# Performance work log

Measured on AMD Instinct MI355X. Metric: run time of the kernel, lower is better.

The kernel has to match this reference:

```python
import jax, jax.numpy as jnp
import numpy as np

B, L, C, H = 4, 2048, 1024, 16
D = C // H
MAX_SCALE_MUL = float(np.log(100.0))
EPS = 1e-12


def setup_inputs() -> dict:
    key = jax.random.key(0)
    ks = jax.random.split(key, 7)
    return {
        "x": jax.random.normal(ks[0], (B, L, C), dtype=jnp.float32),
        "W_qkv": jax.random.normal(ks[1], (3 * C, C), dtype=jnp.float32) * (C ** -0.5),
        "q_bias": jax.random.normal(ks[2], (C,), dtype=jnp.float32) * 0.02,
        "v_bias": jax.random.normal(ks[3], (C,), dtype=jnp.float32) * 0.02,
        "scale_mul_log": jnp.full((1, H, 1, 1), np.log(4.0), dtype=jnp.float32),
        "W_proj": jax.random.normal(ks[4], (C, C), dtype=jnp.float32) * (C ** -0.5),
        "b_proj": jax.random.normal(ks[5], (C,), dtype=jnp.float32) * 0.02,
    }


def reference(x, W_qkv, q_bias, v_bias, scale_mul_log, W_proj, b_proj):
    Bb, Ll, Cc = x.shape
    # fused QKV projection with bias = cat(q_bias, zeros, v_bias)
    bias = jnp.concatenate([q_bias, jnp.zeros_like(q_bias), v_bias])
    qkv = (x @ W_qkv.T + bias).reshape(Bb, Ll, 3, H, D)
    q, k, v = (jnp.transpose(qkv[:, :, i], (0, 2, 1, 3)) for i in range(3))  # [B,H,L,D]
    # L2-norm attention: normalize q,k; learned per-head scale on q (clamped)
    scale_mul = jnp.exp(jnp.minimum(scale_mul_log, MAX_SCALE_MUL))  # [1,H,1,1]
    q = q / jnp.maximum(jnp.linalg.norm(q, axis=-1, keepdims=True), EPS) * scale_mul
    k = k / jnp.maximum(jnp.linalg.norm(k, axis=-1, keepdims=True), EPS)
    # SDPA with scale=1 (attn_l2_norm path), no mask, no dropout (eval)
    scores = jnp.einsum("bhqd,bhkd->bhqk", q, k)
    attn = jax.nn.softmax(scores, axis=-1)
    out = jnp.einsum("bhqk,bhkd->bhqd", attn, v)
    out = jnp.transpose(out, (0, 2, 1, 3)).reshape(Bb, Ll, Cc)
    return out @ W_proj.T + b_proj
```

## Files before the change

### kernel.cpp

```cpp
#include <hip/hip_runtime.h>
#include <hip/hip_bf16.h>


typedef __attribute__((ext_vector_type(8))) short bf16x8;
typedef __attribute__((ext_vector_type(4))) float f32x4;
typedef __attribute__((ext_vector_type(16))) float f32x16;

#define MAXLOG 4.60517018598809f
#define LOG2E  1.4426950408889634f

__device__ __forceinline__ float bf2f(unsigned short u) {
    union { unsigned int i; float f; } v; v.i = ((unsigned int)u) << 16; return v.f;
}
__device__ __forceinline__ unsigned short f2bf(float f) {
    union { float f; unsigned int i; } v; v.f = f;
    unsigned int x = v.i;
    return (unsigned short)((x + 0x7FFFu + ((x >> 16) & 1u)) >> 16);
}
__device__ __forceinline__ unsigned fbits(float f) {
    union { float f; unsigned u; } v; v.f = f; return v.u;
}
__device__ __forceinline__ bf16x8 pack8(const float* __restrict__ p) {
    float4 a = *(const float4*)p;
    float4 b = *(const float4*)(p + 4);
    bf16x8 r;
    r[0] = (short)f2bf(a.x); r[1] = (short)f2bf(a.y);
    r[2] = (short)f2bf(a.z); r[3] = (short)f2bf(a.w);
    r[4] = (short)f2bf(b.x); r[5] = (short)f2bf(b.y);
    r[6] = (short)f2bf(b.z); r[7] = (short)f2bf(b.w);
    return r;
}
__device__ __forceinline__ void gload_lds16(const void* g, void* l) {
    __builtin_amdgcn_global_load_lds((const __attribute__((address_space(1))) void*)g,
                                     (__attribute__((address_space(3))) void*)l, 16, 0, 0);
}

__global__ __launch_bounds__(256) void k_prep(
    const float* __restrict__ x, const float* __restrict__ Wqkv,
    const float* __restrict__ Wp, const float* __restrict__ qbia,
    const float* __restrict__ vbia,
    unsigned short* __restrict__ xb, unsigned short* __restrict__ Wqkvb,
    unsigned short* __restrict__ Wpb, float* __restrict__ bias3)
{
    int i = blockIdx.x * 256 + threadIdx.x;
    if (i < 1048576) {
        *(bf16x8*)&xb[(long)i * 8] = pack8(&x[(long)i * 8]);
    } else if (i < 1441792) {
        int j = i - 1048576;
        *(bf16x8*)&Wqkvb[(long)j * 8] = pack8(&Wqkv[(long)j * 8]);
    } else if (i < 1572864) {
        int j = i - 1441792;
        *(bf16x8*)&Wpb[(long)j * 8] = pack8(&Wp[(long)j * 8]);
    } else if (i < 1573248) {
        int j = (i - 1572864) * 8;
        for (int u = 0; u < 8; ++u) {
            int n = j + u;
            float v = 0.0f;
            if (n < 1024) v = qbia[n];
            else if (n >= 2048) v = vbia[n - 2048];
            bias3[n] = v;
        }
    }
}

template<bool OUT_F32>
__global__ __launch_bounds__(256) void k_gemm_lds(
    const unsigned short* __restrict__ A, const unsigned short* __restrict__ Bh,
    const float* __restrict__ bias, void* __restrict__ Cp, int N, int K)
{
    __shared__ unsigned short As[128 * 32];
    __shared__ unsigned short Bs[128 * 32];
    const int t = threadIdx.x, wave = t >> 6, lane = t & 63;
    const int quad = lane >> 4, l16 = lane & 15;
    const int bm = blockIdx.x * 128, bn = blockIdx.y * 128;
    const int wr = (wave >> 1) * 64, wc = (wave & 1) * 64;
    f32x4 acc[4][4] = {};

    const int srow = lane >> 2;
    const int scol = (lane & 3) * 8;
    const int c0 = wave * 2, c1 = wave * 2 + 1;
    const long ga0 = (long)(bm + c0 * 16 + srow) * K + scol;
    const long ga1 = (long)(bm + c1 * 16 + srow) * K + scol;
    const long gb0 = (long)(bn + c0 * 16 + srow) * K + scol;
    const long gb1 = (long)(bn + c1 * 16 + srow) * K + scol;

    for (int kt = 0; kt < K; kt += 32) {
        __syncthreads();
        gload_lds16(&A[ga0 + kt], &As[c0 * 512]);
        gload_lds16(&A[ga1 + kt], &As[c1 * 512]);
        gload_lds16(&Bh[gb0 + kt], &Bs[c0 * 512]);
        gload_lds16(&Bh[gb1 + kt], &Bs[c1 * 512]);
        __syncthreads();
        bf16x8 af[4], bfr[4];
        for (int i = 0; i < 4; ++i)
            af[i] = *(const bf16x8*)&As[(wr + i * 16 + l16) * 32 + quad * 8];
        for (int j = 0; j < 4; ++j)
            bfr[j] = *(const bf16x8*)&Bs[(wc + j * 16 + l16) * 32 + quad * 8];
        for (int i = 0; i < 4; ++i)
            for (int j = 0; j < 4; ++j)
                acc[i][j] = __builtin_amdgcn_mfma_f32_16x16x32_bf16(af[i], bfr[j], acc[i][j], 0, 0, 0);
    }
    for (int j = 0; j < 4; ++j) {
        int gn = bn + wc + j * 16 + l16;
        float bv = bias[gn];
        for (int i = 0; i < 4; ++i) {
            int gm0 = bm + wr + i * 16 + quad * 4;
            for (int r = 0; r < 4; ++r) {
                float val = acc[i][j][r] + bv;
                if (OUT_F32) ((float*)Cp)[(long)(gm0 + r) * N + gn] = val;
                else ((unsigned short*)Cp)[(long)(gm0 + r) * N + gn] = f2bf(val);
            }
        }
    }
}

__global__ __launch_bounds__(256) void k_prep_kv(
    const unsigned short* __restrict__ qkv, unsigned short* __restrict__ kb,
    unsigned short* __restrict__ vT)
{
    __shared__ unsigned short Vsh[64 * 72];
    const int t = threadIdx.x;
    const int bh = blockIdx.y, l0 = blockIdx.x * 64;
    const int h = bh & 15, b = bh >> 4;
    const int ll = t >> 2, c16 = (t & 3) * 16;
    const long rowbase = (long)(b * 2048 + l0 + ll) * 3072;

    {
        bf16x8 k0 = *(const bf16x8*)&qkv[rowbase + 1024 + h * 64 + c16];
        bf16x8 k1 = *(const bf16x8*)&qkv[rowbase + 1024 + h * 64 + c16 + 8];
        float e[16]; float ss = 0.f;
        for (int j = 0; j < 8; ++j) { e[j]     = bf2f((unsigned short)k0[j]); ss += e[j] * e[j]; }
        for (int j = 0; j < 8; ++j) { e[8 + j] = bf2f((unsigned short)k1[j]); ss += e[8 + j] * e[8 + j]; }
        ss += __shfl_xor(ss, 1, 64);
        ss += __shfl_xor(ss, 2, 64);
        float rs = 1.0f / fmaxf(sqrtf(ss), 1e-12f);
        bf16x8 o0, o1;
        for (int j = 0; j < 8; ++j) o0[j] = (short)f2bf(e[j] * rs);
        for (int j = 0; j < 8; ++j) o1[j] = (short)f2bf(e[8 + j] * rs);
        long dst = ((long)bh * 2048 + l0 + ll) * 64 + c16;
        *(bf16x8*)&kb[dst]     = o0;
        *(bf16x8*)&kb[dst + 8] = o1;
    }
    *(bf16x8*)&Vsh[ll * 72 + c16]     = *(const bf16x8*)&qkv[rowbase + 2048 + h * 64 + c16];
    *(bf16x8*)&Vsh[ll * 72 + c16 + 8] = *(const bf16x8*)&qkv[rowbase + 2048 + h * 64 + c16 + 8];
    __syncthreads();
    const int d = t >> 2, ls = (t & 3) * 16;
    unsigned short tmp[16];
    for (int j = 0; j < 16; ++j) tmp[j] = Vsh[(ls + j) * 72 + d];
    long dst = (long)(bh * 64 + d) * 2048 + l0 + ls;
    *(bf16x8*)&vT[dst]     = *(bf16x8*)&tmp[0];
    *(bf16x8*)&vT[dst + 8] = *(bf16x8*)&tmp[8];
}

__global__ __launch_bounds__(256, 4) void k_attn32(
    const unsigned short* __restrict__ qkv, const unsigned short* __restrict__ kb,
    const unsigned short* __restrict__ vT, const float* __restrict__ sml,
    unsigned short* __restrict__ attn)
{
    __shared__ unsigned short Ks[2][64 * 72];
    __shared__ unsigned short Vs[2][64 * 72];
    const int t = threadIdx.x, wave = t >> 6, lane = t & 63;
    const int m32 = lane & 31, half = lane >> 5;
    const int bh = blockIdx.y, h = bh & 15, b = bh >> 4;
    const int q0 = blockIdx.x * 128 + wave * 32;
    const float scale = __expf(fminf(sml[h], MAXLOG));
    const float c2 = scale * LOG2E;

    const int qd = m32 >> 2, lo = qd & 3;
    const int prow = ((((lo == 1) || (lo == 2)) ? (qd ^ 3) : qd) << 2) | (m32 & 3);

    bf16x8 aq[4];
    {
        long base = (long)(b * 2048 + q0 + m32) * 3072 + h * 64;
        float e[32]; float ss = 0.f;
        for (int f = 0; f < 4; ++f) {
            aq[f] = *(const bf16x8*)&qkv[base + f * 16 + half * 8];
            for (int j = 0; j < 8; ++j) { float x = bf2f((unsigned short)aq[f][j]); e[f * 8 + j] = x; ss += x * x; }
        }
        ss += __shfl_xor(ss, 32, 64);
        float rs = scale / fmaxf(sqrtf(ss), 1e-12f);
        for (int f = 0; f < 4; ++f)
            for (int j = 0; j < 8; ++j) aq[f][j] = (short)f2bf(e[f * 8 + j] * rs);
    }

    f32x16 o0 = {}, o1 = {}, lacc = {};
    bf16x8 ones; for (int i = 0; i < 8; ++i) ones[i] = (short)0x3F80;
    const int sr = t >> 2, sc = (t & 3) * 16;
    const long kbase = (long)bh * 2048 * 64;
    const long vbase = (long)bh * 64 * 2048;

#define LOADT(kt) \
    kpA = *(const bf16x8*)&kb[kbase + (long)((kt) + sr) * 64 + sc];      \
    kpB = *(const bf16x8*)&kb[kbase + (long)((kt) + sr) * 64 + sc + 8];  \
    vpA = *(const bf16x8*)&vT[vbase + (long)sr * 2048 + (kt) + sc];      \
    vpB = *(const bf16x8*)&vT[vbase + (long)sr * 2048 + (kt) + sc + 8];

#define STORET(buf) \
    *(bf16x8*)&Ks[buf][sr * 72 + sc]     = kpA;  \
    *(bf16x8*)&Ks[buf][sr * 72 + sc + 8] = kpB;  \
    *(bf16x8*)&Vs[buf][sr * 72 + sc]     = vpA;  \
    *(bf16x8*)&Vs[buf][sr * 72 + sc + 8] = vpB;

#define ATTN_STEP(KS, VS) \
    for (int ktile = 0; ktile < 2; ++ktile) {                                             \
        f32x16 s = {};                                                                    \
        for (int f = 0; f < 4; ++f) {                                                     \
            bf16x8 bk = *(const bf16x8*)&KS[(ktile * 32 + prow) * 72 + f * 16 + half * 8];\
            s = __builtin_amdgcn_mfma_f32_32x32x16_bf16(bk, aq[f], s, 0, 0, 0);           \
        }                                                                                 \
        unsigned pu[16];                                                                  \
        for (int j = 0; j < 8; ++j) {                                                     \
            pu[j]     = fbits(__builtin_amdgcn_exp2f(s[j]     * LOG2E - c2));             \
            pu[8 + j] = fbits(__builtin_amdgcn_exp2f(s[8 + j] * LOG2E - c2));             \
        }                                                                                 \
        uint4 a0u, a1u;                                                                   \
        a0u.x = __builtin_amdgcn_perm(pu[1],  pu[0],  0x07060302u);                       \
        a0u.y = __builtin_amdgcn_perm(pu[3],  pu[2],  0x07060302u);                       \
        a0u.z = __builtin_amdgcn_perm(pu[5],  pu[4],  0x07060302u);                       \
        a0u.w = __builtin_amdgcn_perm(pu[7],  pu[6],  0x07060302u);                       \
        a1u.x = __builtin_amdgcn_perm(pu[9],  pu[8],  0x07060302u);                       \
        a1u.y = __builtin_amdgcn_perm(pu[11], pu[10], 0x07060302u);                       \
        a1u.z = __builtin_amdgcn_perm(pu[13], pu[12], 0x07060302u);                       \
        a1u.w = __builtin_amdgcn_perm(pu[15], pu[14], 0x07060302u);                       \
        bf16x8 ap0, ap1;                                                                  \
        __builtin_memcpy(&ap0, &a0u, 16); __builtin_memcpy(&ap1, &a1u, 16);               \
        for (int c = 0; c < 2; ++c) {                                                     \
            bf16x8 apc = c ? ap1 : ap0;                                                   \
            bf16x8 bv0 = *(const bf16x8*)&VS[m32 * 72        + ktile * 32 + c * 16 + half * 8]; \
            bf16x8 bv1 = *(const bf16x8*)&VS[(32 + m32) * 72 + ktile * 32 + c * 16 + half * 8]; \
            o0   = __builtin_amdgcn_mfma_f32_32x32x16_bf16(apc, bv0, o0, 0, 0, 0);        \
            o1   = __builtin_amdgcn_mfma_f32_32x32x16_bf16(apc, bv1, o1, 0, 0, 0);        \
            lacc = __builtin_amdgcn_mfma_f32_32x32x16_bf16(apc, ones, lacc, 0, 0, 0);     \
        }                                                                                 \
    }

    bf16x8 kpA, kpB, vpA, vpB;
    LOADT(0)
    STORET(0)
    __syncthreads();

    for (int kt = 0; kt < 2048; kt += 128) {
        LOADT(kt + 64)
        ATTN_STEP(Ks[0], Vs[0])
        STORET(1)
        __syncthreads();
        const bool more = (kt + 128) < 2048;
        if (more) { LOADT(kt + 128) }
        ATTN_STEP(Ks[1], Vs[1])
        if (more) {
            STORET(0)
            __syncthreads();
        }
    }
#undef LOADT
#undef STORET
#undef ATTN_STEP

    for (int r = 0; r < 16; ++r) {
        int m = (r & 3) + 8 * (r >> 2) + 4 * half;
        float inv = 1.0f / lacc[r];
        long dst = (long)(b * 2048 + q0 + m) * 1024 + h * 64;
        attn[dst + m32]      = f2bf(o0[r] * inv);
        attn[dst + 32 + m32] = f2bf(o1[r] * inv);
    }
}

extern "C" void kernel_launch(void* const* d_in, const int* in_sizes, int n_in,
                              void* d_out, int out_size, void* d_ws, size_t ws_size,
                              hipStream_t stream) {
    const float* x    = (const float*)d_in[0];
    const float* Wqkv = (const float*)d_in[1];
    const float* qbia = (const float*)d_in[2];
    const float* vbia = (const float*)d_in[3];
    const float* sml  = (const float*)d_in[4];
    const float* Wp   = (const float*)d_in[5];
    const float* bp   = (const float*)d_in[6];

    char* ws = (char*)d_ws;
    unsigned short* qkv   = (unsigned short*)ws;
    unsigned short* kbuf  = (unsigned short*)(ws + 50331648);
    unsigned short* Wqkvb = kbuf;
    unsigned short* vT    = (unsigned short*)(ws + 67108864);
    unsigned short* xb    = vT;
    unsigned short* attnb = (unsigned short*)(ws + 83886080);
    float*          bias3 = (float*)(ws + 100663296);
    unsigned short* Wpb   = (unsigned short*)(ws + 100679680);
    float*          out   = (float*)d_out;

    hipLaunchKernelGGL(k_prep, dim3(6146), dim3(256), 0, stream,
                       x, Wqkv, Wp, qbia, vbia, xb, Wqkvb, Wpb, bias3);
    hipLaunchKernelGGL((k_gemm_lds<false>), dim3(64, 24), dim3(256), 0, stream,
                       xb, Wqkvb, bias3, (void*)qkv, 3072, 1024);
    hipLaunchKernelGGL(k_prep_kv, dim3(32, 64), dim3(256), 0, stream, qkv, kbuf, vT);
    hipLaunchKernelGGL(k_attn32, dim3(16, 64), dim3(256), 0, stream, qkv, kbuf, vT, sml, attnb);
    hipLaunchKernelGGL((k_gemm_lds<true>), dim3(64, 8), dim3(256), 0, stream,
                       attnb, Wpb, bp, (void*)out, 1024, 1024);
}
```

Baseline: 299.0 us.

## Use 32x32 MFMA in GEMM, fold log2e into q, split score accumulators

The projection GEMM moves from 16x16x32 MFMA tiles to 32x32x16 tiles with a 2x2 accumulator layout per wave, which cuts LDS fragment reads per MFMA. In attention, log2(e) is folded into the normalized q scale so the exp2 argument needs no per-element multiply. The max subtraction is skipped when the scale is small, since scores are bounded by the scale after L2 normalization. The QK dot product now uses two independent accumulators to shorten the MFMA dependency chain. Rounding log2e into bf16 q adds a small precision cost.

```diff
diff --git a/kernel.cpp b/kernel.cpp
--- a/kernel.cpp
+++ b/kernel.cpp
@@ -3,7 +3,6 @@
 
 
 typedef __attribute__((ext_vector_type(8))) short bf16x8;
-typedef __attribute__((ext_vector_type(4))) float f32x4;
 typedef __attribute__((ext_vector_type(16))) float f32x16;
 
 #define MAXLOG 4.60517018598809f
@@ -71,10 +70,10 @@
     __shared__ unsigned short As[128 * 32];
     __shared__ unsigned short Bs[128 * 32];
     const int t = threadIdx.x, wave = t >> 6, lane = t & 63;
-    const int quad = lane >> 4, l16 = lane & 15;
+    const int m32 = lane & 31, half = lane >> 5;
     const int bm = blockIdx.x * 128, bn = blockIdx.y * 128;
     const int wr = (wave >> 1) * 64, wc = (wave & 1) * 64;
-    f32x4 acc[4][4] = {};
+    f32x16 acc[2][2] = {};
 
     const int srow = lane >> 2;
     const int scol = (lane & 3) * 8;
@@ -91,27 +90,30 @@
         gload_lds16(&Bh[gb0 + kt], &Bs[c0 * 512]);
         gload_lds16(&Bh[gb1 + kt], &Bs[c1 * 512]);
         __syncthreads();
-        bf16x8 af[4], bfr[4];
-        for (int i = 0; i < 4; ++i)
-            af[i] = *(const bf16x8*)&As[(wr + i * 16 + l16) * 32 + quad * 8];
-        for (int j = 0; j < 4; ++j)
-            bfr[j] = *(const bf16x8*)&Bs[(wc + j * 16 + l16) * 32 + quad * 8];
-        for (int i = 0; i < 4; ++i)
-            for (int j = 0; j < 4; ++j)
-                acc[i][j] = __builtin_amdgcn_mfma_f32_16x16x32_bf16(af[i], bfr[j], acc[i][j], 0, 0, 0);
-    }
-    for (int j = 0; j < 4; ++j) {
-        int gn = bn + wc + j * 16 + l16;
-        float bv = bias[gn];
-        for (int i = 0; i < 4; ++i) {
-            int gm0 = bm + wr + i * 16 + quad * 4;
-            for (int r = 0; r < 4; ++r) {
-                float val = acc[i][j][r] + bv;
-                if (OUT_F32) ((float*)Cp)[(long)(gm0 + r) * N + gn] = val;
-                else ((unsigned short*)Cp)[(long)(gm0 + r) * N + gn] = f2bf(val);
+        bf16x8 af[2][2], bfr[2][2];
+        for (int mt = 0; mt < 2; ++mt)
+            for (int f = 0; f < 2; ++f)
+                af[mt][f] = *(const bf16x8*)&As[(wr + mt * 32 + m32) * 32 + f * 16 + half * 8];
+        for (int nt = 0; nt < 2; ++nt)
+            for (int f = 0; f < 2; ++f)
+                bfr[nt][f] = *(const bf16x8*)&Bs[(wc + nt * 32 + m32) * 32 + f * 16 + half * 8];
+        for (int f = 0; f < 2; ++f)
+            for (int mt = 0; mt < 2; ++mt)
+                for (int nt = 0; nt < 2; ++nt)
+                    acc[mt][nt] = __builtin_amdgcn_mfma_f32_32x32x16_bf16(
+                        af[mt][f], bfr[nt][f], acc[mt][nt], 0, 0, 0);
+    }
+    for (int mt = 0; mt < 2; ++mt)
+        for (int nt = 0; nt < 2; ++nt) {
+            int gn = bn + wc + nt * 32 + m32;
+            float bv = bias[gn];
+            for (int r = 0; r < 16; ++r) {
+                int gm = bm + wr + mt * 32 + (r & 3) + 8 * (r >> 2) + 4 * half;
+                float val = acc[mt][nt][r] + bv;
+                if (OUT_F32) ((float*)Cp)[(long)gm * N + gn] = val;
+                else ((unsigned short*)Cp)[(long)gm * N + gn] = f2bf(val);
             }
         }
-    }
 }
 
 __global__ __launch_bounds__(256) void k_prep_kv(
@@ -178,7 +180,7 @@
             for (int j = 0; j < 8; ++j) { float x = bf2f((unsigned short)aq[f][j]); e[f * 8 + j] = x; ss += x * x; }
         }
         ss += __shfl_xor(ss, 32, 64);
-        float rs = scale / fmaxf(sqrtf(ss), 1e-12f);
+        float rs = (scale * LOG2E) / fmaxf(sqrtf(ss), 1e-12f);
         for (int f = 0; f < 4; ++f)
             for (int j = 0; j < 8; ++j) aq[f][j] = (short)f2bf(e[f * 8 + j] * rs);
     }
@@ -201,37 +203,55 @@
     *(bf16x8*)&Vs[buf][sr * 72 + sc]     = vpA;  \
     *(bf16x8*)&Vs[buf][sr * 72 + sc + 8] = vpB;
 
-#define ATTN_STEP(KS, VS) \
-    for (int ktile = 0; ktile < 2; ++ktile) {                                             \
-        f32x16 s = {};                                                                    \
-        for (int f = 0; f < 4; ++f) {                                                     \
-            bf16x8 bk = *(const bf16x8*)&KS[(ktile * 32 + prow) * 72 + f * 16 + half * 8];\
-            s = __builtin_amdgcn_mfma_f32_32x32x16_bf16(bk, aq[f], s, 0, 0, 0);           \
-        }                                                                                 \
-        unsigned pu[16];                                                                  \
-        for (int j = 0; j < 8; ++j) {                                                     \
-            pu[j]     = fbits(__builtin_amdgcn_exp2f(s[j]     * LOG2E - c2));             \
-            pu[8 + j] = fbits(__builtin_amdgcn_exp2f(s[8 + j] * LOG2E - c2));             \
-        }                                                                                 \
-        uint4 a0u, a1u;                                                                   \
-        a0u.x = __builtin_amdgcn_perm(pu[1],  pu[0],  0x07060302u);                       \
-        a0u.y = __builtin_amdgcn_perm(pu[3],  pu[2],  0x07060302u);                       \
-        a0u.z = __builtin_amdgcn_perm(pu[5],  pu[4],  0x07060302u);                       \
-        a0u.w = __builtin_amdgcn_perm(pu[7],  pu[6],  0x07060302u);                       \
-        a1u.x = __builtin_amdgcn_perm(pu[9],  pu[8],  0x07060302u);                       \
-        a1u.y = __builtin_amdgcn_perm(pu[11], pu[10], 0x07060302u);                       \
-        a1u.z = __builtin_amdgcn_perm(pu[13], pu[12], 0x07060302u);                       \
-        a1u.w = __builtin_amdgcn_perm(pu[15], pu[14], 0x07060302u);                       \
-        bf16x8 ap0, ap1;                                                                  \
-        __builtin_memcpy(&ap0, &a0u, 16); __builtin_memcpy(&ap1, &a1u, 16);               \
-        for (int c = 0; c < 2; ++c) {                                                     \
-            bf16x8 apc = c ? ap1 : ap0;                                                   \
+#define ATTN_STEP(KS, VS, SUB) \
+    for (int ktile = 0; ktile < 2; ++ktile) {                                              \
+        const unsigned short* krow = &KS[(ktile * 32 + prow) * 72 + half * 8];             \
+        bf16x8 bk0 = *(const bf16x8*)&krow[0];                                             \
+        bf16x8 bk1 = *(const bf16x8*)&krow[16];                                            \
+        bf16x8 bk2 = *(const bf16x8*)&krow[32];                                            \
+        bf16x8 bk3 = *(const bf16x8*)&krow[48];                                            \
+        f32x16 sa = {}, sb = {};                                                           \
+        sa = __builtin_amdgcn_mfma_f32_32x32x16_bf16(bk0, aq[0], sa, 0, 0, 0);             \
+        sb = __builtin_amdgcn_mfma_f32_32x32x16_bf16(bk2, aq[2], sb, 0, 0, 0);             \
+        sa = __builtin_amdgcn_mfma_f32_32x32x16_bf16(bk1, aq[1], sa, 0, 0, 0);             \
+        sb = __builtin_amdgcn_mfma_f32_32x32x16_bf16(bk3, aq[3], sb, 0, 0, 0);             \
+        unsigned pu[16];                                                                   \
+        for (int j = 0; j < 16; ++j)                                                       \
+            pu[j] = fbits(__builtin_amdgcn_exp2f(sa[j] + sb[j] - (SUB)));                  \
+        uint4 a0u, a1u;                                                                    \
+        a0u.x = __builtin_amdgcn_perm(pu[1],  pu[0],  0x07060302u);                        \
+        a0u.y = __builtin_amdgcn_perm(pu[3],  pu[2],  0x07060302u);                        \
+        a0u.z = __builtin_amdgcn_perm(pu[5],  pu[4],  0x07060302u);                        \
+        a0u.w = __builtin_amdgcn_perm(pu[7],  pu[6],  0x07060302u);                        \
+        a1u.x = __builtin_amdgcn_perm(pu[9],  pu[8],  0x07060302u);                        \
+        a1u.y = __builtin_amdgcn_perm(pu[11], pu[10], 0x07060302u);                        \
+        a1u.z = __builtin_amdgcn_perm(pu[13], pu[12], 0x07060302u);                        \
+        a1u.w = __builtin_amdgcn_perm(pu[15], pu[14], 0x07060302u);                        \
+        bf16x8 ap0, ap1;                                                                   \
+        __builtin_memcpy(&ap0, &a0u, 16); __builtin_memcpy(&ap1, &a1u, 16);                \
+        for (int c = 0; c < 2; ++c) {                                                      \
+            bf16x8 apc = c ? ap1 : ap0;                                                    \
             bf16x8 bv0 = *(const bf16x8*)&VS[m32 * 72        + ktile * 32 + c * 16 + half * 8]; \
             bf16x8 bv1 = *(const bf16x8*)&VS[(32 + m32) * 72 + ktile * 32 + c * 16 + half * 8]; \
-            o0   = __builtin_amdgcn_mfma_f32_32x32x16_bf16(apc, bv0, o0, 0, 0, 0);        \
-            o1   = __builtin_amdgcn_mfma_f32_32x32x16_bf16(apc, bv1, o1, 0, 0, 0);        \
-            lacc = __builtin_amdgcn_mfma_f32_32x32x16_bf16(apc, ones, lacc, 0, 0, 0);     \
-        }                                                                                 \
+            o0   = __builtin_amdgcn_mfma_f32_32x32x16_bf16(apc, bv0, o0, 0, 0, 0);         \
+            o1   = __builtin_amdgcn_mfma_f32_32x32x16_bf16(apc, bv1, o1, 0, 0, 0);         \
+            lacc = __builtin_amdgcn_mfma_f32_32x32x16_bf16(apc, ones, lacc, 0, 0, 0);      \
+        }                                                                                  \
+    }
+
+#define KLOOP(SUB) \
+    for (int kt = 0; kt < 2048; kt += 128) {                 \
+        LOADT(kt + 64)                                       \
+        ATTN_STEP(Ks[0], Vs[0], SUB)                         \
+        STORET(1)                                            \
+        __syncthreads();                                     \
+        const bool more = (kt + 128) < 2048;                 \
+        if (more) { LOADT(kt + 128) }                        \
+        ATTN_STEP(Ks[1], Vs[1], SUB)                         \
+        if (more) {                                          \
+            STORET(0)                                        \
+            __syncthreads();                                 \
+        }                                                    \
     }
 
     bf16x8 kpA, kpB, vpA, vpB;
@@ -239,22 +259,15 @@
     STORET(0)
     __syncthreads();
 
-    for (int kt = 0; kt < 2048; kt += 128) {
-        LOADT(kt + 64)
-        ATTN_STEP(Ks[0], Vs[0])
-        STORET(1)
-        __syncthreads();
-        const bool more = (kt + 128) < 2048;
-        if (more) { LOADT(kt + 128) }
-        ATTN_STEP(Ks[1], Vs[1])
-        if (more) {
-            STORET(0)
-            __syncthreads();
-        }
+    if (c2 < 30.0f) {
+        KLOOP(0.0f)
+    } else {
+        KLOOP(c2)
     }
 #undef LOADT
 #undef STORET
 #undef ATTN_STEP
+#undef KLOOP
 
     for (int r = 0; r < 16; ++r) {
         int m = (r & 3) + 8 * (r >> 2) + 4 * half;
```

New measurement: 335.2 us. 12.1% more time.
